# Kernel tuning notes

Hardware: AMD Instinct MI355X
Metric: run time of the kernel (lower is better)

The kernel has to match this reference:

```python
import jax, jax.numpy as jnp
import numpy as np

BATCH = 262144
WIN = 5
VOCAB = 100000
EMB = 50
HID = 250
OUT = 36


def setup_inputs() -> dict:
    key = jax.random.key(0)
    k1, k2, k3, k4, k5, k6 = jax.random.split(key, 6)
    idx = jax.random.randint(k1, (BATCH, WIN), 0, VOCAB, dtype=jnp.int64 if jax.config.jax_enable_x64 else jnp.int32)
    emb_table = jax.random.normal(k2, (VOCAB, EMB), dtype=jnp.float32) * 0.1
    w_in = jax.random.normal(k3, (WIN * EMB, HID), dtype=jnp.float32) * (1.0 / np.sqrt(WIN * EMB))
    b_in = jax.random.normal(k4, (HID,), dtype=jnp.float32) * 0.01
    w_out = jax.random.normal(k5, (HID, OUT), dtype=jnp.float32) * (1.0 / np.sqrt(HID))
    b_out = jax.random.normal(k6, (OUT,), dtype=jnp.float32) * 0.01
    return {"idx": idx, "emb_table": emb_table, "w_in": w_in, "b_in": b_in, "w_out": w_out, "b_out": b_out}


def reference(idx, emb_table, w_in, b_in, w_out, b_out):
    # Gather window embeddings; indices that are -1 or >= vocab map to zero vectors
    vocab = emb_table.shape[0]
    valid = (idx >= 0) & (idx < vocab)                       # [B, W]
    safe = jnp.clip(idx, 0, vocab - 1)
    emb = emb_table[safe] * valid[..., None].astype(emb_table.dtype)  # [B, W, E]
    x = emb.reshape(emb.shape[0], -1)                        # [B, W*E] concat
    h = jnp.tanh(x @ w_in + b_in)                            # [B, HID]
    return h @ w_out + b_out                                 # [B, OUT]
```

## Files before the change

### kernel.cpp

```cpp
#include <hip/hip_runtime.h>
#include <hip/hip_bf16.h>

#define TPB 256
#define PREP_TPB 256

constexpr int B_    = 262144;
constexpr int WIN_  = 5;
constexpr int VOCAB_= 100000;
constexpr int EMB_  = 50;
constexpr int HID_  = 250;
constexpr int OUT_  = 36;
constexpr int KP    = 256;
constexpr int NP    = 256;
constexpr int OP    = 48;
constexpr int BM    = 64;
constexpr int K1    = 320;
constexpr int ROWB  = 640;

constexpr float TWO_LOG2E = 2.8853900817779268f;

typedef __attribute__((ext_vector_type(8))) short fragA;
typedef __attribute__((ext_vector_type(4))) float fragC;

__device__ __forceinline__ short f2b(float f) {
    __hip_bfloat16 h = __float2bfloat16(f);
    return *reinterpret_cast<short*>(&h);
}

__device__ __forceinline__ unsigned pack2(float x, float y) {
    return (unsigned)(unsigned short)f2b(x) | ((unsigned)(unsigned short)f2b(y) << 16);
}

__device__ __forceinline__ float tanh_b(float a, float b2) {
    float e = __builtin_amdgcn_exp2f(__builtin_fmaf(a, TWO_LOG2E, b2));
    return __builtin_fmaf(-2.f, __builtin_amdgcn_rcpf(e + 1.f), 1.f);
}

__device__ __forceinline__ void* xp(char* xs, int row, int b) {
    return xs + row * ROWB + (b ^ ((row & 7) << 4));
}

__global__ void prep_emb(const float* __restrict__ emb, short* __restrict__ emb_b) {
    int id = blockIdx.x * PREP_TPB + threadIdx.x;
    if (id >= (VOCAB_ + 1) * 32) return;
    int row = id >> 5, c2 = id & 31;
    unsigned v = 0u;
    if (row < VOCAB_ && c2 < 25) {
        float2 f = *(const float2*)(emb + row * EMB_ + 2 * c2);
        v = pack2(f.x, f.y);
    }
    ((unsigned*)emb_b)[id] = v;
}

__global__ void prep_weights(const float* __restrict__ w_in,
                             const float* __restrict__ w_out,
                             const float* __restrict__ b_in,
                             const float* __restrict__ b_out,
                             short* __restrict__ wT,
                             short* __restrict__ woT,
                             float* __restrict__ b_in_p,
                             float* __restrict__ b_out_p) {
    int id = blockIdx.x * PREP_TPB + threadIdx.x;
    if (id < 10 * NP * 32) {
        int kk = id / (NP * 32), r = id - kk * NP * 32;
        int n = r >> 5, j = r & 31;
        int k1 = kk * 32 + j;
        int w = k1 >> 6, e = k1 & 63;
        float v = (n < HID_ && e < EMB_) ? w_in[(w * EMB_ + e) * HID_ + n] : 0.f;
        wT[id] = f2b(v);
        return;
    }
    int id2 = id - 10 * NP * 32;
    if (id2 < 8 * OP * 32) {
        int kk = id2 / (OP * 32), r = id2 - kk * OP * 32;
        int o = r >> 5, j = r & 31;
        int k = kk * 32 + j;
        float v = (o < OUT_ && k < HID_) ? w_out[k * OUT_ + o] : 0.f;
        woT[id2] = f2b(v);
        return;
    }
    int id3 = id2 - 8 * OP * 32;
    if (id3 < NP) { b_in_p[id3] = (id3 < HID_) ? b_in[id3] * TWO_LOG2E : 0.f; return; }
    int id4 = id3 - NP;
    if (id4 < OP) { b_out_p[id4] = (id4 < OUT_) ? b_out[id4] : 0.f; }
}

template<bool BF>
__launch_bounds__(TPB, 4)
__global__ void tagger_main(const int* __restrict__ idx,
                            const float* __restrict__ emb,
                            const short* __restrict__ emb_b,
                            const float* __restrict__ b_in_p,
                            const float* __restrict__ b_out_p,
                            const short* __restrict__ wT,
                            const short* __restrict__ woT,
                            float* __restrict__ out) {
    __shared__ char xs[BM * ROWB];

    const int tid   = threadIdx.x;
    const int lane  = tid & 63;
    const int wave  = tid >> 6;
    const int l16   = lane & 15;
    const int khalf = lane >> 4;
    const int r0    = blockIdx.x * BM;

    if constexpr (BF) {
        #pragma unroll
        for (int it = 0; it < 10; ++it) {
            int o    = (it * TPB + tid) * 16;
            int row  = o / ROWB;
            int bs   = o - row * ROWB;
            int win  = bs >> 7;
            int boff = (bs & 127) ^ ((row & 7) << 4);
            int iv   = idx[(r0 + row) * WIN_ + win];
            unsigned safe = ((unsigned)iv < (unsigned)VOCAB_) ? (unsigned)iv : (unsigned)VOCAB_;
            const short* src = emb_b + (size_t)safe * 64 + (boff >> 1);
            __builtin_amdgcn_global_load_lds(
                (const __attribute__((address_space(1))) unsigned int*)src,
                (__attribute__((address_space(3))) unsigned int*)(xs + it * (TPB * 16) + wave * 1024),
                16, 0, 0);
        }
    } else {
        const int sub = tid & 3;
        #pragma unroll
        for (int it = 0; it < 5; ++it) {
            int p = it * 64 + (tid >> 2);
            int row = p / 5, win = p - row * 5;
            int iv  = idx[r0 * WIN_ + p];
            bool valid = (iv >= 0 && iv < VOCAB_);
            const float* base = emb + (valid ? iv : 0) * EMB_;
            #pragma unroll
            for (int j = 0; j < 7; ++j) {
                int ch = sub + 4 * j;
                if (ch < 25) {
                    float2 v = make_float2(0.f, 0.f);
                    if (valid) v = *(const float2*)(base + 2 * ch);
                    *(unsigned*)xp(xs, row, win * 128 + 4 * ch) = pack2(v.x, v.y);
                }
            }
            for (int ch = 25 + sub; ch < 32; ch += 4)
                *(unsigned*)xp(xs, row, win * 128 + 4 * ch) = 0u;
        }
    }
    __syncthreads();

    fragC acc[4][4];
    #pragma unroll
    for (int mf = 0; mf < 4; ++mf)
        #pragma unroll
        for (int nf = 0; nf < 4; ++nf)
            acc[mf][nf] = (fragC){0.f, 0.f, 0.f, 0.f};

    const int nb = wave * 64;
    const short* wbase = wT + (nb + l16) * 32 + khalf * 8;

    #pragma unroll 2
    for (int kk = 0; kk < 10; ++kk) {
        fragA a[4], b[4];
        #pragma unroll
        for (int mf = 0; mf < 4; ++mf)
            a[mf] = *(const fragA*)xp(xs, mf * 16 + l16, kk * 64 + khalf * 16);
        #pragma unroll
        for (int nf = 0; nf < 4; ++nf)
            b[nf] = *(const fragA*)(wbase + kk * (NP * 32) + nf * (16 * 32));
        #pragma unroll
        for (int mf = 0; mf < 4; ++mf)
            #pragma unroll
            for (int nf = 0; nf < 4; ++nf)
                acc[mf][nf] = __builtin_amdgcn_mfma_f32_16x16x32_bf16(b[nf], a[mf], acc[mf][nf], 0, 0, 0);
    }

    __syncthreads();

    #pragma unroll
    for (int nf = 0; nf < 4; ++nf) {
        const int n0 = nb + nf * 16 + khalf * 4;
        const float4 bi = *(const float4*)&b_in_p[n0];
        #pragma unroll
        for (int mf = 0; mf < 4; ++mf) {
            const int row = mf * 16 + l16;
            uint2 v;
            v.x = pack2(tanh_b(acc[mf][nf][0], bi.x), tanh_b(acc[mf][nf][1], bi.y));
            v.y = pack2(tanh_b(acc[mf][nf][2], bi.z), tanh_b(acc[mf][nf][3], bi.w));
            *(uint2*)xp(xs, row, 2 * n0) = v;
        }
    }
    __syncthreads();

    fragC acc2[3];
    #pragma unroll
    for (int of = 0; of < 3; ++of) acc2[of] = (fragC){0.f, 0.f, 0.f, 0.f};

    const short* wobase = woT + l16 * 32 + khalf * 8;

    #pragma unroll 2
    for (int kk = 0; kk < 8; ++kk) {
        fragA ha = *(const fragA*)xp(xs, wave * 16 + l16, 64 * kk + 16 * khalf);
        #pragma unroll
        for (int of = 0; of < 3; ++of) {
            fragA wb = *(const fragA*)(wobase + kk * (OP * 32) + of * (16 * 32));
            acc2[of] = __builtin_amdgcn_mfma_f32_16x16x32_bf16(wb, ha, acc2[of], 0, 0, 0);
        }
    }

    {
        const int row = r0 + wave * 16 + l16;
        #pragma unroll
        for (int of = 0; of < 3; ++of) {
            const int o0 = of * 16 + khalf * 4;
            if (o0 < OUT_) {
                const float4 bo = *(const float4*)&b_out_p[o0];
                float4 v;
                v.x = acc2[of][0] + bo.x;
                v.y = acc2[of][1] + bo.y;
                v.z = acc2[of][2] + bo.z;
                v.w = acc2[of][3] + bo.w;
                *(float4*)&out[row * OUT_ + o0] = v;
            }
        }
    }
}

extern "C" void kernel_launch(void* const* d_in, const int* in_sizes, int n_in,
                              void* d_out, int out_size, void* d_ws, size_t ws_size,
                              hipStream_t stream) {
    const int*   idx   = (const int*)d_in[0];
    const float* emb   = (const float*)d_in[1];
    const float* w_in  = (const float*)d_in[2];
    const float* b_in  = (const float*)d_in[3];
    const float* w_out = (const float*)d_in[4];
    const float* b_out = (const float*)d_in[5];
    float* out = (float*)d_out;

    const size_t emb_b_elems = (size_t)(VOCAB_ + 1) * 64;
    const size_t tail_elems  = (size_t)10 * NP * 32 + 8 * OP * 32 + 2 * (NP + OP);
    const size_t need_bf = (emb_b_elems + tail_elems + 256) * 2;
    const bool bf = (ws_size >= need_bf);

    short* emb_b = nullptr;
    short* wT;
    if (bf) {
        emb_b = (short*)d_ws;
        wT    = emb_b + emb_b_elems;
        prep_emb<<<((VOCAB_ + 1) * 32 + PREP_TPB - 1) / PREP_TPB, PREP_TPB, 0, stream>>>(emb, emb_b);
    } else {
        wT = (short*)d_ws;
    }
    short* woT = wT + 10 * NP * 32;
    float* b_in_p  = (float*)(woT + 8 * OP * 32);
    float* b_out_p = b_in_p + NP;

    int prep_threads = 10 * NP * 32 + 8 * OP * 32 + NP + OP;
    prep_weights<<<(prep_threads + PREP_TPB - 1) / PREP_TPB, PREP_TPB, 0, stream>>>(
        w_in, w_out, b_in, b_out, wT, woT, b_in_p, b_out_p);

    if (bf)
        tagger_main<true><<<B_ / BM, TPB, 0, stream>>>(idx, emb, emb_b, b_in_p, b_out_p, wT, woT, out);
    else
        tagger_main<false><<<B_ / BM, TPB, 0, stream>>>(idx, emb, emb_b, b_in_p, b_out_p, wT, woT, out);
}
```

Baseline: 91.98 us.

## Reorganize LDS layout by window and overlap embedding gather with GEMM1 k-steps

Changes the shared-memory layout of the gathered embeddings to be window-major (one 8 KB slab per window), so each pair of k-steps depends only on a subset of the async global-to-LDS loads. Index loads are hoisted and issued first, then all ten async gathers are launched, and the first GEMM proceeds in phases that each wait on a partial vmcnt plus a barrier. Earlier k-steps can then start while later windows are still in flight. The hidden-layer buffer is re-addressed with a 512-byte row stride. The added barriers and manual waitcnt scheduling rely on the async loads completing in issue order.

```diff
diff --git a/kernel.cpp b/kernel.cpp
--- a/kernel.cpp
+++ b/kernel.cpp
@@ -15,7 +15,6 @@
 constexpr int OP    = 48;
 constexpr int BM    = 64;
 constexpr int K1    = 320;
-constexpr int ROWB  = 640;
 
 constexpr float TWO_LOG2E = 2.8853900817779268f;
 
@@ -34,10 +33,6 @@
 __device__ __forceinline__ float tanh_b(float a, float b2) {
     float e = __builtin_amdgcn_exp2f(__builtin_fmaf(a, TWO_LOG2E, b2));
     return __builtin_fmaf(-2.f, __builtin_amdgcn_rcpf(e + 1.f), 1.f);
-}
-
-__device__ __forceinline__ void* xp(char* xs, int row, int b) {
-    return xs + row * ROWB + (b ^ ((row & 7) << 4));
 }
 
 __global__ void prep_emb(const float* __restrict__ emb, short* __restrict__ emb_b) {
@@ -85,6 +80,28 @@
     if (id4 < OP) { b_out_p[id4] = (id4 < OUT_) ? b_out[id4] : 0.f; }
 }
 
+#define KSTEP(kk) { \
+    fragA a_[4], b_[4]; \
+    constexpr int win_ = (kk) >> 1, half_ = (kk) & 1; \
+    _Pragma("unroll") \
+    for (int mf = 0; mf < 4; ++mf) \
+        a_[mf] = *(const fragA*)(xs + win_ * 8192 + (mf * 16 + l16) * 128 + \
+                                 ((half_ * 64 + khalf * 16) ^ ((l16 & 7) << 4))); \
+    _Pragma("unroll") \
+    for (int nf = 0; nf < 4; ++nf) \
+        b_[nf] = *(const fragA*)(wbase + (kk) * (NP * 32) + nf * (16 * 32)); \
+    _Pragma("unroll") \
+    for (int mf = 0; mf < 4; ++mf) \
+        _Pragma("unroll") \
+        for (int nf = 0; nf < 4; ++nf) \
+            acc[mf][nf] = __builtin_amdgcn_mfma_f32_16x16x32_bf16(b_[nf], a_[mf], acc[mf][nf], 0, 0, 0); }
+
+#define PHASE(VM, K0, K1) \
+    asm volatile("s_waitcnt vmcnt(" #VM ")" ::: "memory"); \
+    __builtin_amdgcn_s_barrier(); \
+    __builtin_amdgcn_sched_barrier(0); \
+    KSTEP(K0); KSTEP(K1);
+
 template<bool BF>
 __launch_bounds__(TPB, 4)
 __global__ void tagger_main(const int* __restrict__ idx,
@@ -95,7 +112,7 @@
                             const short* __restrict__ wT,
                             const short* __restrict__ woT,
                             float* __restrict__ out) {
-    __shared__ char xs[BM * ROWB];
+    __shared__ char xs[40960];
 
     const int tid   = threadIdx.x;
     const int lane  = tid & 63;
@@ -104,22 +121,40 @@
     const int khalf = lane >> 4;
     const int r0    = blockIdx.x * BM;
 
+    const int nb = wave * 64;
+    const short* wbase = wT + (nb + l16) * 32 + khalf * 8;
+
+    fragC acc[4][4];
+    #pragma unroll
+    for (int mf = 0; mf < 4; ++mf)
+        #pragma unroll
+        for (int nf = 0; nf < 4; ++nf)
+            acc[mf][nf] = (fragC){0.f, 0.f, 0.f, 0.f};
+
     if constexpr (BF) {
+        const short* src[10];
         #pragma unroll
         for (int it = 0; it < 10; ++it) {
-            int o    = (it * TPB + tid) * 16;
-            int row  = o / ROWB;
-            int bs   = o - row * ROWB;
-            int win  = bs >> 7;
-            int boff = (bs & 127) ^ ((row & 7) << 4);
-            int iv   = idx[(r0 + row) * WIN_ + win];
+            const int win = it >> 1, row = (it & 1) * 32 + (tid >> 3), sub = tid & 7;
+            int iv = idx[(r0 + row) * WIN_ + win];
             unsigned safe = ((unsigned)iv < (unsigned)VOCAB_) ? (unsigned)iv : (unsigned)VOCAB_;
-            const short* src = emb_b + (size_t)safe * 64 + (boff >> 1);
+            src[it] = emb_b + (size_t)safe * 64 + ((((unsigned)sub * 16) ^ (((unsigned)row & 7) << 4)) >> 1);
+        }
+        asm volatile("s_waitcnt vmcnt(0)" ::: "memory");
+        __builtin_amdgcn_sched_barrier(0);
+        #pragma unroll
+        for (int it = 0; it < 10; ++it) {
             __builtin_amdgcn_global_load_lds(
-                (const __attribute__((address_space(1))) unsigned int*)src,
-                (__attribute__((address_space(3))) unsigned int*)(xs + it * (TPB * 16) + wave * 1024),
+                (const __attribute__((address_space(1))) unsigned int*)src[it],
+                (__attribute__((address_space(3))) unsigned int*)(xs + it * 4096 + wave * 1024),
                 16, 0, 0);
-        }
+            __builtin_amdgcn_sched_barrier(0);
+        }
+        PHASE(8, 0, 1)
+        PHASE(6, 2, 3)
+        PHASE(4, 4, 5)
+        PHASE(2, 6, 7)
+        PHASE(0, 8, 9)
     } else {
         const int sub = tid & 3;
         #pragma unroll
@@ -129,45 +164,23 @@
             int iv  = idx[r0 * WIN_ + p];
             bool valid = (iv >= 0 && iv < VOCAB_);
             const float* base = emb + (valid ? iv : 0) * EMB_;
+            char* wrow = xs + win * 8192 + row * 128;
+            const int swz = (row & 7) << 4;
             #pragma unroll
             for (int j = 0; j < 7; ++j) {
                 int ch = sub + 4 * j;
                 if (ch < 25) {
                     float2 v = make_float2(0.f, 0.f);
                     if (valid) v = *(const float2*)(base + 2 * ch);
-                    *(unsigned*)xp(xs, row, win * 128 + 4 * ch) = pack2(v.x, v.y);
+                    *(unsigned*)(wrow + ((4 * ch) ^ swz)) = pack2(v.x, v.y);
                 }
             }
             for (int ch = 25 + sub; ch < 32; ch += 4)
-                *(unsigned*)xp(xs, row, win * 128 + 4 * ch) = 0u;
-        }
-    }
-    __syncthreads();
-
-    fragC acc[4][4];
-    #pragma unroll
-    for (int mf = 0; mf < 4; ++mf)
-        #pragma unroll
-        for (int nf = 0; nf < 4; ++nf)
-            acc[mf][nf] = (fragC){0.f, 0.f, 0.f, 0.f};
-
-    const int nb = wave * 64;
-    const short* wbase = wT + (nb + l16) * 32 + khalf * 8;
-
-    #pragma unroll 2
-    for (int kk = 0; kk < 10; ++kk) {
-        fragA a[4], b[4];
-        #pragma unroll
-        for (int mf = 0; mf < 4; ++mf)
-            a[mf] = *(const fragA*)xp(xs, mf * 16 + l16, kk * 64 + khalf * 16);
-        #pragma unroll
-        for (int nf = 0; nf < 4; ++nf)
-            b[nf] = *(const fragA*)(wbase + kk * (NP * 32) + nf * (16 * 32));
-        #pragma unroll
-        for (int mf = 0; mf < 4; ++mf)
-            #pragma unroll
-            for (int nf = 0; nf < 4; ++nf)
-                acc[mf][nf] = __builtin_amdgcn_mfma_f32_16x16x32_bf16(b[nf], a[mf], acc[mf][nf], 0, 0, 0);
+                *(unsigned*)(wrow + ((4 * ch) ^ swz)) = 0u;
+        }
+        __syncthreads();
+        KSTEP(0) KSTEP(1) KSTEP(2) KSTEP(3) KSTEP(4)
+        KSTEP(5) KSTEP(6) KSTEP(7) KSTEP(8) KSTEP(9)
     }
 
     __syncthreads();
@@ -182,7 +195,7 @@
             uint2 v;
             v.x = pack2(tanh_b(acc[mf][nf][0], bi.x), tanh_b(acc[mf][nf][1], bi.y));
             v.y = pack2(tanh_b(acc[mf][nf][2], bi.z), tanh_b(acc[mf][nf][3], bi.w));
-            *(uint2*)xp(xs, row, 2 * n0) = v;
+            *(uint2*)(xs + row * 512 + ((2 * n0) ^ ((l16 & 7) << 4))) = v;
         }
     }
     __syncthreads();
@@ -195,7 +208,8 @@
 
     #pragma unroll 2
     for (int kk = 0; kk < 8; ++kk) {
-        fragA ha = *(const fragA*)xp(xs, wave * 16 + l16, 64 * kk + 16 * khalf);
+        const int row = wave * 16 + l16;
+        fragA ha = *(const fragA*)(xs + row * 512 + ((kk * 64 + khalf * 16) ^ ((l16 & 7) << 4)));
         #pragma unroll
         for (int of = 0; of < 3; ++of) {
             fragA wb = *(const fragA*)(wobase + kk * (OP * 32) + of * (16 * 32));
```

After: 94.58 us. +2.8%, slower.

## Double block tile to 128 rows with 8 waves in a 2x4 grid

Applied to the files above, without the earlier changes.

Raises threads per block to 512 and rows per block to 128. The first GEMM's waves now form a 2x4 grid over rows and hidden columns, so each weight fragment loaded from global memory serves twice as many rows. The hidden-layer tile in shared memory now uses a 512-byte row stride with XOR swizzling. The second GEMM is split into 24 (row-fragment, output-fragment) tasks spread across the 8 waves. This halves the number of blocks and the per-row weight traffic, but doubles LDS per block (80KB) and keeps launch bounds at 4 blocks per SM, which may cut occupancy.

```diff
diff --git a/kernel.cpp b/kernel.cpp
--- a/kernel.cpp
+++ b/kernel.cpp
@@ -1,7 +1,7 @@
 #include <hip/hip_runtime.h>
 #include <hip/hip_bf16.h>
 
-#define TPB 256
+#define TPB 512
 #define PREP_TPB 256
 
 constexpr int B_    = 262144;
@@ -13,7 +13,7 @@
 constexpr int KP    = 256;
 constexpr int NP    = 256;
 constexpr int OP    = 48;
-constexpr int BM    = 64;
+constexpr int BM    = 128;
 constexpr int K1    = 320;
 constexpr int ROWB  = 640;
 
@@ -100,6 +100,8 @@
     const int tid   = threadIdx.x;
     const int lane  = tid & 63;
     const int wave  = tid >> 6;
+    const int wm    = wave >> 2;
+    const int wn    = wave & 3;
     const int l16   = lane & 15;
     const int khalf = lane >> 4;
     const int r0    = blockIdx.x * BM;
@@ -124,7 +126,7 @@
         const int sub = tid & 3;
         #pragma unroll
         for (int it = 0; it < 5; ++it) {
-            int p = it * 64 + (tid >> 2);
+            int p = it * 128 + (tid >> 2);
             int row = p / 5, win = p - row * 5;
             int iv  = idx[r0 * WIN_ + p];
             bool valid = (iv >= 0 && iv < VOCAB_);
@@ -151,7 +153,8 @@
         for (int nf = 0; nf < 4; ++nf)
             acc[mf][nf] = (fragC){0.f, 0.f, 0.f, 0.f};
 
-    const int nb = wave * 64;
+    const int nb    = wn * 64;
+    const int mbase = wm * 64;
     const short* wbase = wT + (nb + l16) * 32 + khalf * 8;
 
     #pragma unroll 2
@@ -159,7 +162,7 @@
         fragA a[4], b[4];
         #pragma unroll
         for (int mf = 0; mf < 4; ++mf)
-            a[mf] = *(const fragA*)xp(xs, mf * 16 + l16, kk * 64 + khalf * 16);
+            a[mf] = *(const fragA*)xp(xs, mbase + mf * 16 + l16, kk * 64 + khalf * 16);
         #pragma unroll
         for (int nf = 0; nf < 4; ++nf)
             b[nf] = *(const fragA*)(wbase + kk * (NP * 32) + nf * (16 * 32));
@@ -178,45 +181,39 @@
         const float4 bi = *(const float4*)&b_in_p[n0];
         #pragma unroll
         for (int mf = 0; mf < 4; ++mf) {
-            const int row = mf * 16 + l16;
+            const int row = mbase + mf * 16 + l16;
             uint2 v;
             v.x = pack2(tanh_b(acc[mf][nf][0], bi.x), tanh_b(acc[mf][nf][1], bi.y));
             v.y = pack2(tanh_b(acc[mf][nf][2], bi.z), tanh_b(acc[mf][nf][3], bi.w));
-            *(uint2*)xp(xs, row, 2 * n0) = v;
+            *(uint2*)(xs + row * 512 + ((2 * n0) ^ ((l16 & 7) << 4))) = v;
         }
     }
     __syncthreads();
 
-    fragC acc2[3];
+    const short* wobase = woT + l16 * 32 + khalf * 8;
+
     #pragma unroll
-    for (int of = 0; of < 3; ++of) acc2[of] = (fragC){0.f, 0.f, 0.f, 0.f};
-
-    const short* wobase = woT + l16 * 32 + khalf * 8;
-
-    #pragma unroll 2
-    for (int kk = 0; kk < 8; ++kk) {
-        fragA ha = *(const fragA*)xp(xs, wave * 16 + l16, 64 * kk + 16 * khalf);
-        #pragma unroll
-        for (int of = 0; of < 3; ++of) {
+    for (int i = 0; i < 3; ++i) {
+        const int t  = wave + 8 * i;
+        const int rf = t & 7, of = t >> 3;
+        fragC acc2 = (fragC){0.f, 0.f, 0.f, 0.f};
+        #pragma unroll 2
+        for (int kk = 0; kk < 8; ++kk) {
+            const int row = rf * 16 + l16;
+            fragA ha = *(const fragA*)(xs + row * 512 + ((kk * 64 + khalf * 16) ^ ((l16 & 7) << 4)));
             fragA wb = *(const fragA*)(wobase + kk * (OP * 32) + of * (16 * 32));
-            acc2[of] = __builtin_amdgcn_mfma_f32_16x16x32_bf16(wb, ha, acc2[of], 0, 0, 0);
-        }
-    }
-
-    {
-        const int row = r0 + wave * 16 + l16;
-        #pragma unroll
-        for (int of = 0; of < 3; ++of) {
-            const int o0 = of * 16 + khalf * 4;
-            if (o0 < OUT_) {
-                const float4 bo = *(const float4*)&b_out_p[o0];
-                float4 v;
-                v.x = acc2[of][0] + bo.x;
-                v.y = acc2[of][1] + bo.y;
-                v.z = acc2[of][2] + bo.z;
-                v.w = acc2[of][3] + bo.w;
-                *(float4*)&out[row * OUT_ + o0] = v;
-            }
+            acc2 = __builtin_amdgcn_mfma_f32_16x16x32_bf16(wb, ha, acc2, 0, 0, 0);
+        }
+        const int o0 = of * 16 + khalf * 4;
+        if (o0 < OUT_) {
+            const int row = r0 + rf * 16 + l16;
+            const float4 bo = *(const float4*)&b_out_p[o0];
+            float4 v;
+            v.x = acc2[0] + bo.x;
+            v.y = acc2[1] + bo.y;
+            v.z = acc2[2] + bo.z;
+            v.w = acc2[3] + bo.w;
+            *(float4*)&out[row * OUT_ + o0] = v;
         }
     }
 }
```

Result: slower. 101.1 us (+9.9%).

## Restructure LDS tile to per-window slabs, fully unroll GEMM loops, add MFMA priority

Applied to the files above, without the earlier changes.

The shared-memory input tile now holds one 8 KB slab per window, each with 128-byte rows and an XOR swizzle. The async gather writes directly into these slabs using a simpler address calculation. The hidden activations reuse the buffer with a 512-byte row stride. Both MFMA loops are fully unrolled, and s_setprio is raised around the MFMA bursts so waves issuing matrix ops get scheduling priority over waves issuing loads. The full unroll may increase register pressure under the 4-blocks-per-SM launch bound.

```diff
diff --git a/kernel.cpp b/kernel.cpp
--- a/kernel.cpp
+++ b/kernel.cpp
@@ -14,8 +14,6 @@
 constexpr int NP    = 256;
 constexpr int OP    = 48;
 constexpr int BM    = 64;
-constexpr int K1    = 320;
-constexpr int ROWB  = 640;
 
 constexpr float TWO_LOG2E = 2.8853900817779268f;
 
@@ -34,10 +32,6 @@
 __device__ __forceinline__ float tanh_b(float a, float b2) {
     float e = __builtin_amdgcn_exp2f(__builtin_fmaf(a, TWO_LOG2E, b2));
     return __builtin_fmaf(-2.f, __builtin_amdgcn_rcpf(e + 1.f), 1.f);
-}
-
-__device__ __forceinline__ void* xp(char* xs, int row, int b) {
-    return xs + row * ROWB + (b ^ ((row & 7) << 4));
 }
 
 __global__ void prep_emb(const float* __restrict__ emb, short* __restrict__ emb_b) {
@@ -95,7 +89,7 @@
                             const short* __restrict__ wT,
                             const short* __restrict__ woT,
                             float* __restrict__ out) {
-    __shared__ char xs[BM * ROWB];
+    __shared__ char xs[40960];
 
     const int tid   = threadIdx.x;
     const int lane  = tid & 63;
@@ -107,17 +101,17 @@
     if constexpr (BF) {
         #pragma unroll
         for (int it = 0; it < 10; ++it) {
-            int o    = (it * TPB + tid) * 16;
-            int row  = o / ROWB;
-            int bs   = o - row * ROWB;
-            int win  = bs >> 7;
-            int boff = (bs & 127) ^ ((row & 7) << 4);
-            int iv   = idx[(r0 + row) * WIN_ + win];
+            const int win = it >> 1;
+            const int row = (it & 1) * 32 + (tid >> 3);
+            const int sub = tid & 7;
+            int iv = idx[(r0 + row) * WIN_ + win];
             unsigned safe = ((unsigned)iv < (unsigned)VOCAB_) ? (unsigned)iv : (unsigned)VOCAB_;
-            const short* src = emb_b + (size_t)safe * 64 + (boff >> 1);
+            const short* src = emb_b + (size_t)safe * 64 +
+                               ((((unsigned)sub * 16) ^ (((unsigned)row & 7) << 4)) >> 1);
             __builtin_amdgcn_global_load_lds(
                 (const __attribute__((address_space(1))) unsigned int*)src,
-                (__attribute__((address_space(3))) unsigned int*)(xs + it * (TPB * 16) + wave * 1024),
+                (__attribute__((address_space(3))) unsigned int*)
+                    (xs + win * 8192 + (it & 1) * 4096 + wave * 1024),
                 16, 0, 0);
         }
     } else {
@@ -129,17 +123,19 @@
             int iv  = idx[r0 * WIN_ + p];
             bool valid = (iv >= 0 && iv < VOCAB_);
             const float* base = emb + (valid ? iv : 0) * EMB_;
+            char* wrow = xs + win * 8192 + row * 128;
+            const int swz = (row & 7) << 4;
             #pragma unroll
             for (int j = 0; j < 7; ++j) {
                 int ch = sub + 4 * j;
                 if (ch < 25) {
                     float2 v = make_float2(0.f, 0.f);
                     if (valid) v = *(const float2*)(base + 2 * ch);
-                    *(unsigned*)xp(xs, row, win * 128 + 4 * ch) = pack2(v.x, v.y);
+                    *(unsigned*)(wrow + ((4 * ch) ^ swz)) = pack2(v.x, v.y);
                 }
             }
             for (int ch = 25 + sub; ch < 32; ch += 4)
-                *(unsigned*)xp(xs, row, win * 128 + 4 * ch) = 0u;
+                *(unsigned*)(wrow + ((4 * ch) ^ swz)) = 0u;
         }
     }
     __syncthreads();
@@ -154,20 +150,26 @@
     const int nb = wave * 64;
     const short* wbase = wT + (nb + l16) * 32 + khalf * 8;
 
-    #pragma unroll 2
+    #pragma unroll
     for (int kk = 0; kk < 10; ++kk) {
+        const int win = kk >> 1, half = kk & 1;
         fragA a[4], b[4];
         #pragma unroll
-        for (int mf = 0; mf < 4; ++mf)
-            a[mf] = *(const fragA*)xp(xs, mf * 16 + l16, kk * 64 + khalf * 16);
+        for (int mf = 0; mf < 4; ++mf) {
+            const int row = mf * 16 + l16;
+            a[mf] = *(const fragA*)(xs + win * 8192 + row * 128 +
+                                    ((half * 64 + khalf * 16) ^ ((row & 7) << 4)));
+        }
         #pragma unroll
         for (int nf = 0; nf < 4; ++nf)
             b[nf] = *(const fragA*)(wbase + kk * (NP * 32) + nf * (16 * 32));
+        __builtin_amdgcn_s_setprio(1);
         #pragma unroll
         for (int mf = 0; mf < 4; ++mf)
             #pragma unroll
             for (int nf = 0; nf < 4; ++nf)
                 acc[mf][nf] = __builtin_amdgcn_mfma_f32_16x16x32_bf16(b[nf], a[mf], acc[mf][nf], 0, 0, 0);
+        __builtin_amdgcn_s_setprio(0);
     }
 
     __syncthreads();
@@ -182,7 +184,7 @@
             uint2 v;
             v.x = pack2(tanh_b(acc[mf][nf][0], bi.x), tanh_b(acc[mf][nf][1], bi.y));
             v.y = pack2(tanh_b(acc[mf][nf][2], bi.z), tanh_b(acc[mf][nf][3], bi.w));
-            *(uint2*)xp(xs, row, 2 * n0) = v;
+            *(uint2*)(xs + row * 512 + ((2 * n0) ^ ((row & 7) << 4))) = v;
         }
     }
     __syncthreads();
@@ -193,14 +195,20 @@
 
     const short* wobase = woT + l16 * 32 + khalf * 8;
 
-    #pragma unroll 2
+    #pragma unroll
     for (int kk = 0; kk < 8; ++kk) {
-        fragA ha = *(const fragA*)xp(xs, wave * 16 + l16, 64 * kk + 16 * khalf);
-        #pragma unroll
-        for (int of = 0; of < 3; ++of) {
-            fragA wb = *(const fragA*)(wobase + kk * (OP * 32) + of * (16 * 32));
-            acc2[of] = __builtin_amdgcn_mfma_f32_16x16x32_bf16(wb, ha, acc2[of], 0, 0, 0);
-        }
+        const int row = wave * 16 + l16;
+        fragA ha = *(const fragA*)(xs + row * 512 +
+                                   ((kk * 64 + khalf * 16) ^ ((row & 7) << 4)));
+        fragA wb[3];
+        #pragma unroll
+        for (int of = 0; of < 3; ++of)
+            wb[of] = *(const fragA*)(wobase + kk * (OP * 32) + of * (16 * 32));
+        __builtin_amdgcn_s_setprio(1);
+        #pragma unroll
+        for (int of = 0; of < 3; ++of)
+            acc2[of] = __builtin_amdgcn_mfma_f32_16x16x32_bf16(wb[of], ha, acc2[of], 0, 0, 0);
+        __builtin_amdgcn_s_setprio(0);
     }
 
     {
```

New measurement: 91.67 us. No clear change (-0.3%).
